# Kernel optimization log

Measured on AMD Instinct MI355X. Metric: run time of the kernel, lower is better.

Reference implementation:

```python
import jax, jax.numpy as jnp
import numpy as np

N_NODES = 100000
N_EDGES = 1600000
D_FEAT = 64
D_HID = 128
N_HOP = 3


def setup_inputs() -> dict:
    key = jax.random.key(0)
    ks = jax.random.split(key, 7)
    nodes = jax.random.normal(ks[0], (N_NODES, D_FEAT), dtype=jnp.float32)
    senders = jax.random.randint(ks[1], (N_EDGES,), 0, N_NODES, dtype=jnp.int32)
    receivers = jax.random.randint(ks[2], (N_EDGES,), 0, N_NODES, dtype=jnp.int32)
    # per-hop MLP params (n_hop=3 independent layers), lecun-style scaling
    W1 = jax.random.normal(ks[3], (N_HOP, D_FEAT, D_HID), dtype=jnp.float32) / np.sqrt(D_FEAT)
    b1 = jnp.zeros((N_HOP, D_HID), dtype=jnp.float32)
    W2 = jax.random.normal(ks[4], (N_HOP, D_HID, D_FEAT), dtype=jnp.float32) / np.sqrt(D_HID)
    b2 = jnp.zeros((N_HOP, D_FEAT), dtype=jnp.float32)
    return {"nodes": nodes, "senders": senders, "receivers": receivers,
            "W1": W1, "b1": b1, "W2": W2, "b2": b2}


def _gcn_hop(x, senders, receivers, w1, b1, w2, b2):
    # update_node_fn: 2-layer MLP with leaky_relu between layers
    x = jax.nn.leaky_relu(jnp.dot(x, w1) + b1)
    x = jnp.dot(x, w2) + b2
    n = x.shape[0]
    ones = jnp.ones(senders.shape, dtype=x.dtype)
    send_deg = jax.ops.segment_sum(ones, senders, num_segments=n)
    recv_deg = jax.ops.segment_sum(ones, receivers, num_segments=n)
    # symmetric normalization: D_s^{-1/2} gather -> scatter-sum -> D_r^{-1/2}
    x = x * jax.lax.rsqrt(jnp.maximum(send_deg, 1.0))[:, None]
    x = jax.ops.segment_sum(x[senders], receivers, num_segments=n)
    x = x * jax.lax.rsqrt(jnp.maximum(recv_deg, 1.0))[:, None]
    return x


def reference(nodes, senders, receivers, W1, b1, W2, b2):
    x = nodes
    for i in range(N_HOP):
        x = _gcn_hop(x, senders, receivers, W1[i], b1[i], W2[i], b2[i])
    return x
```

## Files before the change

kernel.cpp:

```cpp
#include <hip/hip_runtime.h>

#define LRELU_SLOPE 0.01f
#define NBLK_A 512
#define BIN_SZ 256
#define MAXBIN 5120
#define NC2 64

typedef unsigned short ushort_t;
typedef unsigned int uint_t;

typedef float f32x4 __attribute__((ext_vector_type(4)));
typedef short bf16x8 __attribute__((ext_vector_type(8)));
#define MFMA16(a, b, c) __builtin_amdgcn_mfma_f32_16x16x32_bf16(a, b, c, 0, 0, 0)

__device__ inline uint_t f2bf(float f) {
    unsigned u = __float_as_uint(f);
    return (u + 0x7FFFu + ((u >> 16) & 1u)) >> 16;
}

__device__ inline void split2(float v, uint_t& hi, uint_t& lo) {
    hi = f2bf(v);
    float hif = __uint_as_float(hi << 16);
    lo = f2bf(v - hif);
}

__device__ inline float4 bf4_to_f4(ushort4 v) {
    float4 r;
    r.x = __uint_as_float((unsigned)v.x << 16);
    r.y = __uint_as_float((unsigned)v.y << 16);
    r.z = __uint_as_float((unsigned)v.z << 16);
    r.w = __uint_as_float((unsigned)v.w << 16);
    return r;
}

__device__ inline void acc_bf8(uint4 v, float* a) {
    a[0] += __uint_as_float(v.x << 16);
    a[1] += __uint_as_float(v.x & 0xFFFF0000u);
    a[2] += __uint_as_float(v.y << 16);
    a[3] += __uint_as_float(v.y & 0xFFFF0000u);
    a[4] += __uint_as_float(v.z << 16);
    a[5] += __uint_as_float(v.z & 0xFFFF0000u);
    a[6] += __uint_as_float(v.w << 16);
    a[7] += __uint_as_float(v.w & 0xFFFF0000u);
}

__device__ inline void acc_bf8m(uint4 v, float ok, float* a) {
    a[0] = fmaf(__uint_as_float(v.x << 16), ok, a[0]);
    a[1] = fmaf(__uint_as_float(v.x & 0xFFFF0000u), ok, a[1]);
    a[2] = fmaf(__uint_as_float(v.y << 16), ok, a[2]);
    a[3] = fmaf(__uint_as_float(v.y & 0xFFFF0000u), ok, a[3]);
    a[4] = fmaf(__uint_as_float(v.z << 16), ok, a[4]);
    a[5] = fmaf(__uint_as_float(v.z & 0xFFFF0000u), ok, a[5]);
    a[6] = fmaf(__uint_as_float(v.w << 16), ok, a[6]);
    a[7] = fmaf(__uint_as_float(v.w & 0xFFFF0000u), ok, a[7]);
}


__global__ __launch_bounds__(256) void binhist_kernel(const int* __restrict__ keys,
        int* __restrict__ cntA, int cs, int e, int nbins) {
    __shared__ int cnt[512];
    int b = blockIdx.x, t = threadIdx.x;
    for (int i = t; i < nbins; i += 256) cnt[i] = 0;
    __syncthreads();
    int base = b * cs, lim = min(cs, e - base);
    for (int i = t; i < lim; i += 256)
        atomicAdd(&cnt[keys[base + i] >> 8], 1);
    __syncthreads();
    for (int i = t; i < nbins; i += 256) cntA[b * nbins + i] = cnt[i];
}

__global__ __launch_bounds__(512) void binoffA_kernel(const int* __restrict__ cntA,
        int* __restrict__ offT, int* __restrict__ binTot, int nbins) {
    __shared__ int s[NBLK_A];
    int bin = blockIdx.x, t = threadIdx.x;
    int v = cntA[t * nbins + bin];
    s[t] = v;
    __syncthreads();
    for (int off = 1; off < NBLK_A; off <<= 1) {
        int add = (t >= off) ? s[t - off] : 0;
        __syncthreads();
        s[t] += add;
        __syncthreads();
    }
    offT[bin * NBLK_A + t] = s[t] - v;
    if (t == NBLK_A - 1) binTot[bin] = s[t];
}

__global__ __launch_bounds__(512) void scanb_kernel(const int* __restrict__ binTot,
        int* __restrict__ binStart, int nbins) {
    __shared__ int s[512];
    int t = threadIdx.x;
    int v = (t < nbins) ? binTot[t] : 0;
    s[t] = v;
    __syncthreads();
    for (int off = 1; off < 512; off <<= 1) {
        int add = (t >= off) ? s[t - off] : 0;
        __syncthreads();
        s[t] += add;
        __syncthreads();
    }
    if (t < nbins) binStart[t] = s[t] - v;
    if (t == nbins - 1) binStart[nbins] = s[t];
}

__global__ __launch_bounds__(256) void binscat_kernel(const int* __restrict__ keys,
        const int* __restrict__ payload, const int* __restrict__ offT,
        const int* __restrict__ binStart,
        uint2* __restrict__ pairs, int cs, int e, int nbins) {
    __shared__ int cur[512];
    int b = blockIdx.x, t = threadIdx.x;
    for (int i = t; i < nbins; i += 256) cur[i] = offT[i * NBLK_A + b] + binStart[i];
    __syncthreads();
    int base = b * cs, lim = min(cs, e - base);
    for (int i = t; i < lim; i += 256) {
        int k = keys[base + i];
        int pl = payload[base + i];
        int pos = atomicAdd(&cur[k >> 8], 1);
        pairs[pos] = make_uint2((unsigned)k, (unsigned)pl);
    }
}

__global__ __launch_bounds__(256) void binsort_kernel(const uint2* __restrict__ pairs,
        const int* __restrict__ binStart, int* __restrict__ row_start,
        int* __restrict__ bucket, int nbins, int n, int e) {
    __shared__ int cnt[BIN_SZ];
    __shared__ int loc[BIN_SZ];
    __shared__ int buf[MAXBIN];
    int bin = blockIdx.x, t = threadIdx.x;
    int e0 = binStart[bin], e1 = binStart[bin + 1];
    int m = e1 - e0;
    if (m > MAXBIN) m = MAXBIN;
    cnt[t] = 0;
    __syncthreads();
    for (int i = t; i < m; i += 256)
        atomicAdd(&cnt[pairs[e0 + i].x & 255], 1);
    __syncthreads();
    int v = cnt[t];
    int node = bin * BIN_SZ + t;
    loc[t] = v;
    __syncthreads();
    for (int off = 1; off < BIN_SZ; off <<= 1) {
        int add = (t >= off) ? loc[t - off] : 0;
        __syncthreads();
        loc[t] += add;
        __syncthreads();
    }
    int excl = loc[t] - v;
    if (node < n) row_start[node] = e0 + excl;
    if (bin == nbins - 1 && t == 255) row_start[n] = e;
    cnt[t] = excl;
    __syncthreads();
    for (int i = t; i < m; i += 256) {
        uint2 pr = pairs[e0 + i];
        int pos = atomicAdd(&cnt[pr.x & 255], 1);
        buf[pos] = (int)pr.y;
    }
    __syncthreads();
    for (int i = t; i < m; i += 256) bucket[e0 + i] = buf[i];
}


__global__ __launch_bounds__(256) void hist8v2_kernel(const int* __restrict__ keys,
        uint_t* __restrict__ hist, int cs, int e, int half, int nwords) {
    __shared__ uint_t lds[12500];
    int c = blockIdx.x >> 1;
    int h = blockIdx.x & 1;
    int t = threadIdx.x;
    int hw = half >> 2;
    for (int i = t; i < hw; i += 256) lds[i] = 0;
    __syncthreads();
    int base = c * cs, lim = min(cs, e - base);
    int lo = h * half;
    for (int i = t; i < lim; i += 256) {
        int v = keys[base + i] - lo;
        if ((unsigned)v < (unsigned)half)
            atomicAdd(&lds[v >> 2], 1u << ((v & 3) * 8));
    }
    __syncthreads();
    uint_t* d = hist + (size_t)c * nwords + (size_t)h * hw;
    for (int i = t; i < hw; i += 256) d[i] = lds[i];
}

__global__ __launch_bounds__(256) void scancv2_kernel(const uint_t* __restrict__ hist,
        int* __restrict__ deg, int nwords, int n) {
    int w = blockIdx.x * 256 + threadIdx.x;
    if (w >= nwords) return;
    uint_t run = 0;
    for (int c = 0; c < NC2; c++) run += hist[(size_t)c * nwords + w];
    int v = w * 4;
    if (v + 3 < n) {
        ((int4*)deg)[w] = make_int4(run & 255, (run >> 8) & 255,
                                    (run >> 16) & 255, (int)(run >> 24));
    } else {
        for (int j = 0; j < 4 && v + j < n; j++) deg[v + j] = (run >> (8 * j)) & 255;
    }
}


__global__ __launch_bounds__(256) void prep_w_kernel(const float* __restrict__ W1,
        const float* __restrict__ W2, ushort_t* __restrict__ w1p, ushort_t* __restrict__ w2p) {
    int hop = blockIdx.x;
    const float* w1 = W1 + hop * 64 * 128;
    const float* w2 = W2 + hop * 128 * 64;
    ushort_t* p1h = w1p + (size_t)hop * 16384;
    ushort_t* p1l = p1h + 8192;
    ushort_t* p2h = w2p + (size_t)hop * 16384;
    ushort_t* p2l = p2h + 8192;
    for (int i = threadIdx.x; i < 8192; i += 256) {
        int j = i & 7, o = (i >> 3) & 127, cq = i >> 10;
        int k = (cq >> 2) * 32 + (cq & 3) * 8 + j;
        uint_t h, l;
        split2(w1[k * 128 + o], h, l);
        p1h[i] = (ushort_t)h; p1l[i] = (ushort_t)l;
    }
    for (int i = threadIdx.x; i < 8192; i += 256) {
        int j = i & 7, o = (i >> 3) & 63, cq = i >> 9;
        int k = (cq >> 2) * 32 + (cq & 3) * 8 + j;
        uint_t h, l;
        split2(w2[k * 64 + o], h, l);
        p2h[i] = (ushort_t)h; p2l[i] = (ushort_t)l;
    }
}


template<int GATHER>
__global__ __launch_bounds__(512) void fused_mlp_kernel(const float* __restrict__ x,
        const ushort_t* __restrict__ yin, const int* __restrict__ rs,
        const int* __restrict__ bucket,
        const ushort_t* __restrict__ w1p, const float* __restrict__ b1g,
        const ushort_t* __restrict__ w2p, const float* __restrict__ b2g,
        const int* __restrict__ sdeg, ushort_t* __restrict__ y, int n) {
    __shared__ __align__(16) char smem[54272];
    ushort_t* xsh = (ushort_t*)smem;
    ushort_t* xsl = xsh + 4608;
    ushort_t* hsh = xsl + 4608;
    ushort_t* hsl = hsh + 8704;
    float* b1f   = (float*)(hsl + 8704);
    float* b2f   = b1f + 128;
    float* snorm = b2f + 64;
    float* ybuf  = (float*)smem;

    const ushort_t* w1ph = w1p;
    const ushort_t* w1pl = w1p + 8192;
    const ushort_t* w2ph = w2p;
    const ushort_t* w2pl = w2p + 8192;

    int tid = threadIdx.x;
    int nb = blockIdx.x * 64;

    if (tid < 32) ((float4*)b1f)[tid] = ((const float4*)b1g)[tid];
    else if (tid < 48) ((float4*)b2f)[tid - 32] = ((const float4*)b2g)[tid - 32];
    if (tid >= 448) {
        int t = tid - 448;
        int gn = nb + t;
        int d = (gn < n) ? sdeg[gn] : 1;
        snorm[t] = rsqrtf(fmaxf((float)d, 1.0f));
    }

    if (GATHER) {
        int node = tid >> 3, j = tid & 7;
        int gn = nb + node;
        float a[8];
        #pragma unroll
        for (int k = 0; k < 8; k++) a[k] = 0.f;
        if (gn < n) {
            int s0 = rs[gn];
            int deg = rs[gn + 1] - s0;
            const uint4* yrow = (const uint4*)yin;
            int i = 0;
            for (; i + 16 <= deg; i += 16) {
                int idx[16];
                #pragma unroll
                for (int k = 0; k < 16; k++) idx[k] = bucket[s0 + i + k];
                uint4 r0[8];
                #pragma unroll
                for (int k = 0; k < 8; k++) r0[k] = yrow[(size_t)idx[k] * 8 + j];
                #pragma unroll
                for (int k = 0; k < 8; k++) acc_bf8(r0[k], a);
                #pragma unroll
                for (int k = 0; k < 8; k++) r0[k] = yrow[(size_t)idx[8 + k] * 8 + j];
                #pragma unroll
                for (int k = 0; k < 8; k++) acc_bf8(r0[k], a);
            }
            for (; i < deg; i += 8) {
                int idx[8]; float ok[8];
                #pragma unroll
                for (int k = 0; k < 8; k++) {
                    int ii = i + k;
                    bool v = ii < deg;
                    idx[k] = bucket[v ? s0 + ii : s0];
                    ok[k] = v ? 1.0f : 0.0f;
                }
                uint4 rr[8];
                #pragma unroll
                for (int k = 0; k < 8; k++) rr[k] = yrow[(size_t)idx[k] * 8 + j];
                #pragma unroll
                for (int k = 0; k < 8; k++) acc_bf8m(rr[k], ok[k], a);
            }
            float sc = rsqrtf(fmaxf((float)deg, 1.0f));
            #pragma unroll
            for (int k = 0; k < 8; k++) a[k] *= sc;
        }
        uint_t h[8], l[8];
        #pragma unroll
        for (int k = 0; k < 8; k++) split2(a[k], h[k], l[k]);
        uint4 oh, ol;
        oh.x = h[0] | (h[1] << 16); oh.y = h[2] | (h[3] << 16);
        oh.z = h[4] | (h[5] << 16); oh.w = h[6] | (h[7] << 16);
        ol.x = l[0] | (l[1] << 16); ol.y = l[2] | (l[3] << 16);
        ol.z = l[4] | (l[5] << 16); ol.w = l[6] | (l[7] << 16);
        *(uint4*)&xsh[node * 72 + j * 8] = oh;
        *(uint4*)&xsl[node * 72 + j * 8] = ol;
    } else {
        for (int i = tid; i < 1024; i += 512) {
            int node = i >> 4, c4 = i & 15;
            int gn = nb + node;
            float4 v = make_float4(0.f, 0.f, 0.f, 0.f);
            if (gn < n) v = ((const float4*)x)[(size_t)gn * 16 + c4];
            uint_t h0, l0, h1, l1, h2, l2, h3, l3;
            split2(v.x, h0, l0); split2(v.y, h1, l1);
            split2(v.z, h2, l2); split2(v.w, h3, l3);
            *(uint2*)&xsh[node * 72 + c4 * 4] = make_uint2(h0 | (h1 << 16), h2 | (h3 << 16));
            *(uint2*)&xsl[node * 72 + c4 * 4] = make_uint2(l0 | (l1 << 16), l2 | (l3 << 16));
        }
    }
    __syncthreads();

    int w = tid >> 6, lane = tid & 63;
    int q = lane >> 4, m = lane & 15;
    int oq = w & 3, nh = w >> 2;
    bool even = ((m & 1) == 0);

    {
        f32x4 acc[2][2];
        #pragma unroll
        for (int a = 0; a < 2; a++)
            #pragma unroll
            for (int b = 0; b < 2; b++) acc[a][b] = (f32x4)(0.f);

        #pragma unroll
        for (int c = 0; c < 2; c++) {
            bf16x8 Ah[2], Al[2];
            #pragma unroll
            for (int nt = 0; nt < 2; nt++) {
                int node = nh * 32 + nt * 16 + m;
                Ah[nt] = *(const bf16x8*)&xsh[node * 72 + c * 32 + q * 8];
                Al[nt] = *(const bf16x8*)&xsl[node * 72 + c * 32 + q * 8];
            }
            #pragma unroll
            for (int ot = 0; ot < 2; ot++) {
                int o1 = oq * 32 + ot * 16 + m;
                size_t fo = (size_t)((c * 4 + q) * 128 + o1) * 8;
                bf16x8 Bh = *(const bf16x8*)&w1ph[fo];
                bf16x8 Bl = *(const bf16x8*)&w1pl[fo];
                #pragma unroll
                for (int nt = 0; nt < 2; nt++) {
                    acc[ot][nt] = MFMA16(Ah[nt], Bh, acc[ot][nt]);
                    acc[ot][nt] = MFMA16(Ah[nt], Bl, acc[ot][nt]);
                    acc[ot][nt] = MFMA16(Al[nt], Bh, acc[ot][nt]);
                }
            }
        }
        float b1v[2];
        b1v[0] = b1f[oq * 32 + m];
        b1v[1] = b1f[oq * 32 + 16 + m];
        #pragma unroll
        for (int ot = 0; ot < 2; ot++)
            #pragma unroll
            for (int nt = 0; nt < 2; nt++) {
                float hv[4], pv[4];
                #pragma unroll
                for (int r = 0; r < 4; r++) {
                    float t = acc[ot][nt][r] + b1v[ot];
                    hv[r] = (t > 0.f) ? t : LRELU_SLOPE * t;
                }
                #pragma unroll
                for (int r = 0; r < 4; r++) pv[r] = __shfl_xor(hv[r], 1, 64);
                int kpos = oq * 32 + ot * 16 + (m & ~1);
                #pragma unroll
                for (int rr = 0; rr < 2; rr++) {
                    int r = even ? rr : (2 + rr);
                    float vlo = even ? hv[r] : pv[r];
                    float vhi = even ? pv[r] : hv[r];
                    uint_t ah, al, bh, bl;
                    split2(vlo, ah, al);
                    split2(vhi, bh, bl);
                    int node = nh * 32 + nt * 16 + 4 * q + r;
                    *(uint_t*)&hsh[node * 136 + kpos] = ah | (bh << 16);
                    *(uint_t*)&hsl[node * 136 + kpos] = al | (bl << 16);
                }
            }
    }
    __syncthreads();

    {
        int ot2 = oq;
        f32x4 acc2[2];
        acc2[0] = (f32x4)(0.f);
        acc2[1] = (f32x4)(0.f);
        #pragma unroll
        for (int c = 0; c < 4; c++) {
            int o2 = ot2 * 16 + m;
            size_t fo = (size_t)((c * 4 + q) * 64 + o2) * 8;
            bf16x8 Bh = *(const bf16x8*)&w2ph[fo];
            bf16x8 Bl = *(const bf16x8*)&w2pl[fo];
            #pragma unroll
            for (int nt = 0; nt < 2; nt++) {
                int node = nh * 32 + nt * 16 + m;
                bf16x8 Ah = *(const bf16x8*)&hsh[node * 136 + c * 32 + q * 8];
                bf16x8 Al = *(const bf16x8*)&hsl[node * 136 + c * 32 + q * 8];
                acc2[nt] = MFMA16(Ah, Bh, acc2[nt]);
                acc2[nt] = MFMA16(Ah, Bl, acc2[nt]);
                acc2[nt] = MFMA16(Al, Bh, acc2[nt]);
            }
        }
        float b2v = b2f[ot2 * 16 + m];
        #pragma unroll
        for (int nt = 0; nt < 2; nt++)
            #pragma unroll
            for (int r = 0; r < 4; r++) {
                int node = nh * 32 + nt * 16 + 4 * q + r;
                float sn = snorm[node];
                ybuf[node * 68 + ot2 * 16 + m] = (acc2[nt][r] + b2v) * sn;
            }
    }
    __syncthreads();

    {
        int node = tid >> 3, c8 = tid & 7;
        int gn = nb + node;
        if (gn < n) {
            const float* src = &ybuf[node * 68 + c8 * 8];
            float4 v0 = *(const float4*)src;
            float4 v1 = *(const float4*)(src + 4);
            uint4 o;
            o.x = f2bf(v0.x) | (f2bf(v0.y) << 16);
            o.y = f2bf(v0.z) | (f2bf(v0.w) << 16);
            o.z = f2bf(v1.x) | (f2bf(v1.y) << 16);
            o.w = f2bf(v1.z) | (f2bf(v1.w) << 16);
            ((uint4*)y)[(size_t)gn * 8 + c8] = o;
        }
    }
}


__global__ __launch_bounds__(256) void agg_kernel(const ushort_t* __restrict__ y,
        const int* __restrict__ rs, const int* __restrict__ bucket,
        float* __restrict__ dst, int n) {
    int wid  = (blockIdx.x * 256 + threadIdx.x) >> 6;
    int lane = threadIdx.x & 63;
    int nd   = lane >> 5;
    int slot = (lane >> 4) & 1;
    int f4   = lane & 15;
    int node = wid * 2 + nd;
    if (node >= n) return;
    int s0  = rs[node];
    int deg = rs[node + 1] - s0;
    const ushort4* y4 = (const ushort4*)y;
    float4 acc = make_float4(0.f, 0.f, 0.f, 0.f);
    for (int i = slot; i < deg; i += 16) {
        int idx[8]; float ok[8];
        #pragma unroll
        for (int j = 0; j < 8; j++) {
            int ii = i + 2 * j;
            bool v = ii < deg;
            idx[j] = bucket[v ? s0 + ii : s0];
            ok[j] = v ? 1.0f : 0.0f;
        }
        #pragma unroll
        for (int j = 0; j < 8; j++) {
            float4 v4 = bf4_to_f4(y4[(size_t)idx[j] * 16 + f4]);
            acc.x = fmaf(v4.x, ok[j], acc.x);
            acc.y = fmaf(v4.y, ok[j], acc.y);
            acc.z = fmaf(v4.z, ok[j], acc.z);
            acc.w = fmaf(v4.w, ok[j], acc.w);
        }
    }
    acc.x += __shfl_xor(acc.x, 16, 64);
    acc.y += __shfl_xor(acc.y, 16, 64);
    acc.z += __shfl_xor(acc.z, 16, 64);
    acc.w += __shfl_xor(acc.w, 16, 64);
    if (slot == 0) {
        float sc = rsqrtf(fmaxf((float)deg, 1.0f));
        acc.x *= sc; acc.y *= sc; acc.z *= sc; acc.w *= sc;
        ((float4*)dst)[(size_t)node * 16 + f4] = acc;
    }
}


extern "C" void kernel_launch(void* const* d_in, const int* in_sizes, int n_in,
                              void* d_out, int out_size, void* d_ws, size_t ws_size,
                              hipStream_t stream) {
    const float* nodes     = (const float*)d_in[0];
    const int*   senders   = (const int*)d_in[1];
    const int*   receivers = (const int*)d_in[2];
    const float* W1 = (const float*)d_in[3];
    const float* b1 = (const float*)d_in[4];
    const float* W2 = (const float*)d_in[5];
    const float* b2 = (const float*)d_in[6];

    int N = in_sizes[0] / 64;
    int E = in_sizes[1];
    int NBINS = (N + BIN_SZ - 1) / BIN_SZ;
    int CSA = (E + NBLK_A - 1) / NBLK_A;
    int CS2 = (E + NC2 - 1) / NC2;
    int HALF = ((N + 7) / 8) * 4;
    int NW2 = 2 * (HALF >> 2);

    char* p = (char*)d_ws;
    auto carve = [&](size_t bytes) -> char* {
        char* r = p;
        p += (bytes + 255) & ~(size_t)255;
        return r;
    };
    ushort_t* yA   = (ushort_t*)carve((size_t)N * 64 * 2);
    ushort_t* yB   = (ushort_t*)carve((size_t)N * 64 * 2);
    int*      rs   = (int*)carve((size_t)(N + 1) * 4);
    int*      sdeg = (int*)carve((size_t)N * 4);
    int*      bucket = (int*)carve((size_t)E * 4);
    int*      binStart = (int*)carve((size_t)(NBINS + 1) * 4);
    int*      binTot   = (int*)carve((size_t)NBINS * 4);
    ushort_t* w1p  = (ushort_t*)carve((size_t)3 * 16384 * 2);
    ushort_t* w2p  = (ushort_t*)carve((size_t)3 * 16384 * 2);
    char* scratch  = carve((size_t)E * 8 + 2 * (size_t)NBLK_A * NBINS * 4 + 4096);
    uint2* pairs = (uint2*)scratch;
    int*   cntA  = (int*)(scratch + (size_t)E * 8);
    int*   offT  = cntA + (size_t)NBLK_A * NBINS;
    uint_t* T1   = (uint_t*)pairs;

    prep_w_kernel<<<3, 256, 0, stream>>>(W1, W2, w1p, w2p);
    binhist_kernel<<<NBLK_A, 256, 0, stream>>>(receivers, cntA, CSA, E, NBINS);
    binoffA_kernel<<<NBINS, NBLK_A, 0, stream>>>(cntA, offT, binTot, NBINS);
    scanb_kernel<<<1, 512, 0, stream>>>(binTot, binStart, NBINS);
    binscat_kernel<<<NBLK_A, 256, 0, stream>>>(receivers, senders, offT, binStart, pairs, CSA, E, NBINS);
    binsort_kernel<<<NBINS, 256, 0, stream>>>(pairs, binStart, rs, bucket, NBINS, N, E);
    hist8v2_kernel<<<NC2 * 2, 256, 0, stream>>>(senders, T1, CS2, E, HALF, NW2);
    scancv2_kernel<<<(NW2 + 255) / 256, 256, 0, stream>>>(T1, sdeg, NW2, N);

    int mbf = (N + 63) / 64;
    int agg_blocks = (N / 2 + 4) / 4 + 1;

    fused_mlp_kernel<0><<<mbf, 512, 0, stream>>>(nodes, nullptr, nullptr, nullptr,
            w1p, b1, w2p, b2, sdeg, yA, N);
    fused_mlp_kernel<1><<<mbf, 512, 0, stream>>>(nullptr, yA, rs, bucket,
            w1p + 16384, b1 + 128, w2p + 16384, b2 + 64, sdeg, yB, N);
    fused_mlp_kernel<1><<<mbf, 512, 0, stream>>>(nullptr, yB, rs, bucket,
            w1p + 32768, b1 + 256, w2p + 32768, b2 + 128, sdeg, yA, N);
    agg_kernel<<<agg_blocks, 256, 0, stream>>>(yA, rs, bucket, (float*)d_out, N);
}
```

Measured before the change: 365.6 us.

## Drop LDS staging of biases, norms and output; store bf16 directly from MFMA results

Bias and degree-norm values are loaded straight from global memory into registers instead of being staged in shared memory. The final ybuf round-trip and its trailing barrier are removed; each lane writes its bf16 output element directly. This shrinks the shared-memory footprint, adds a min-blocks launch bound hint, and raises the NC2 constant. The direct per-element 2-byte stores are far less coalesced than the previous 16-byte row writes, and the occupancy hint may cause register spills.

```diff
diff --git a/kernel.cpp b/kernel.cpp
--- a/kernel.cpp
+++ b/kernel.cpp
@@ -4,7 +4,7 @@
 #define NBLK_A 512
 #define BIN_SZ 256
 #define MAXBIN 5120
-#define NC2 64
+#define NC2 128
 
 typedef unsigned short ushort_t;
 typedef unsigned int uint_t;
@@ -224,21 +224,17 @@
 
 
 template<int GATHER>
-__global__ __launch_bounds__(512) void fused_mlp_kernel(const float* __restrict__ x,
+__global__ __launch_bounds__(512, 6) void fused_mlp_kernel(const float* __restrict__ x,
         const ushort_t* __restrict__ yin, const int* __restrict__ rs,
         const int* __restrict__ bucket,
         const ushort_t* __restrict__ w1p, const float* __restrict__ b1g,
         const ushort_t* __restrict__ w2p, const float* __restrict__ b2g,
         const int* __restrict__ sdeg, ushort_t* __restrict__ y, int n) {
-    __shared__ __align__(16) char smem[54272];
+    __shared__ __align__(16) char smem[53248];
     ushort_t* xsh = (ushort_t*)smem;
     ushort_t* xsl = xsh + 4608;
     ushort_t* hsh = xsl + 4608;
     ushort_t* hsl = hsh + 8704;
-    float* b1f   = (float*)(hsl + 8704);
-    float* b2f   = b1f + 128;
-    float* snorm = b2f + 64;
-    float* ybuf  = (float*)smem;
 
     const ushort_t* w1ph = w1p;
     const ushort_t* w1pl = w1p + 8192;
@@ -247,15 +243,6 @@
 
     int tid = threadIdx.x;
     int nb = blockIdx.x * 64;
-
-    if (tid < 32) ((float4*)b1f)[tid] = ((const float4*)b1g)[tid];
-    else if (tid < 48) ((float4*)b2f)[tid - 32] = ((const float4*)b2g)[tid - 32];
-    if (tid >= 448) {
-        int t = tid - 448;
-        int gn = nb + t;
-        int d = (gn < n) ? sdeg[gn] : 1;
-        snorm[t] = rsqrtf(fmaxf((float)d, 1.0f));
-    }
 
     if (GATHER) {
         int node = tid >> 3, j = tid & 7;
@@ -332,6 +319,10 @@
     bool even = ((m & 1) == 0);
 
     {
+        float b1v[2];
+        b1v[0] = b1g[oq * 32 + m];
+        b1v[1] = b1g[oq * 32 + 16 + m];
+
         f32x4 acc[2][2];
         #pragma unroll
         for (int a = 0; a < 2; a++)
@@ -361,9 +352,6 @@
                 }
             }
         }
-        float b1v[2];
-        b1v[0] = b1f[oq * 32 + m];
-        b1v[1] = b1f[oq * 32 + 16 + m];
         #pragma unroll
         for (int ot = 0; ot < 2; ot++)
             #pragma unroll
@@ -395,6 +383,18 @@
 
     {
         int ot2 = oq;
+        float b2v = b2g[ot2 * 16 + m];
+        float snv[2][4];
+        #pragma unroll
+        for (int nt = 0; nt < 2; nt++)
+            #pragma unroll
+            for (int r = 0; r < 4; r++) {
+                int node = nh * 32 + nt * 16 + 4 * q + r;
+                int gn = nb + node;
+                int d = (gn < n) ? sdeg[gn] : 1;
+                snv[nt][r] = rsqrtf(fmaxf((float)d, 1.0f));
+            }
+
         f32x4 acc2[2];
         acc2[0] = (f32x4)(0.f);
         acc2[1] = (f32x4)(0.f);
@@ -414,32 +414,17 @@
                 acc2[nt] = MFMA16(Al, Bh, acc2[nt]);
             }
         }
-        float b2v = b2f[ot2 * 16 + m];
         #pragma unroll
         for (int nt = 0; nt < 2; nt++)
             #pragma unroll
             for (int r = 0; r < 4; r++) {
                 int node = nh * 32 + nt * 16 + 4 * q + r;
-                float sn = snorm[node];
-                ybuf[node * 68 + ot2 * 16 + m] = (acc2[nt][r] + b2v) * sn;
-            }
-    }
-    __syncthreads();
-
-    {
-        int node = tid >> 3, c8 = tid & 7;
-        int gn = nb + node;
-        if (gn < n) {
-            const float* src = &ybuf[node * 68 + c8 * 8];
-            float4 v0 = *(const float4*)src;
-            float4 v1 = *(const float4*)(src + 4);
-            uint4 o;
-            o.x = f2bf(v0.x) | (f2bf(v0.y) << 16);
-            o.y = f2bf(v0.z) | (f2bf(v0.w) << 16);
-            o.z = f2bf(v1.x) | (f2bf(v1.y) << 16);
-            o.w = f2bf(v1.z) | (f2bf(v1.w) << 16);
-            ((uint4*)y)[(size_t)gn * 8 + c8] = o;
-        }
+                int gn = nb + node;
+                if (gn < n) {
+                    float v = (acc2[nt][r] + b2v) * snv[nt][r];
+                    y[(size_t)gn * 64 + ot2 * 16 + m] = (ushort_t)f2bf(v);
+                }
+            }
     }
 }
 
```

Result: slower. 415.7 us (+13.7%).
